# Kernel optimization log

Hardware: AMD Instinct MI355X
Metric: run time of the kernel (lower is better)

## Reference

```python
import jax, jax.numpy as jnp
import numpy as np

NUM_CODES = 1024
EMBED_DIM = 256
COMMIT_COST = 0.25


def setup_inputs() -> dict:
    key = jax.random.key(0)
    k1, k2 = jax.random.split(key)
    z_hat = jax.random.normal(k1, (32, EMBED_DIM, 32, 32), dtype=jnp.float32)
    # nn.Embedding weight init: uniform(-1/num_codes, 1/num_codes)
    embedding_weight = jax.random.uniform(
        k2, (NUM_CODES, EMBED_DIM), dtype=jnp.float32,
        minval=-1.0 / NUM_CODES, maxval=1.0 / NUM_CODES)
    return {"z_hat": z_hat, "embedding_weight": embedding_weight}


def reference(z_hat, embedding_weight):
    B, C, H, W = z_hat.shape
    # [B,C,H,W] -> [B,H,W,C] -> [N,C]
    z = jnp.transpose(z_hat, (0, 2, 3, 1))
    z_flat = z.reshape(-1, C)
    # squared L2 distances via expansion: ||z||^2 + ||e||^2 - 2 z.e
    dists = (jnp.sum(z_flat ** 2, axis=1, keepdims=True)
             + jnp.sum(embedding_weight ** 2, axis=1)
             - 2.0 * jnp.matmul(z_flat, embedding_weight.T))  # [N, K]
    idx = jnp.argmin(dists, axis=1)                            # [N]
    z_q = embedding_weight[idx].reshape(B, H, W, C)
    sg = jax.lax.stop_gradient
    codebook_loss = jnp.mean((z_q - sg(z)) ** 2)
    commitment_loss = COMMIT_COST * jnp.mean((z - sg(z_q)) ** 2)
    # straight-through estimator
    z_q_ste = z + sg(z_q - z)
    z_q_ste = jnp.transpose(z_q_ste, (0, 3, 1, 2))             # [B,C,H,W]
    indices = idx.reshape(B, H, W)
    return (z_q_ste, codebook_loss, commitment_loss, indices)
```

## Files before the change

kernel.cpp:

```cpp
#include <hip/hip_runtime.h>

#define NUM_CODES 1024
#define EMBED_DIM 256
#define NPIX      32768
#define NELEM     8388608

#define LOSS_OFF 8388608
#define IDX_OFF  8388610
#define EH_F     4194304
#define ESQ_F    4325376
#define ZSQ_F    4326400

#define MARGIN   1.0e-3f
#define CAP      16

typedef _Float16 half_t;
typedef _Float16 half8 __attribute__((ext_vector_type(8)));
typedef _Float16 half4 __attribute__((ext_vector_type(4)));
typedef float    f32x4 __attribute__((ext_vector_type(4)));
typedef unsigned int u32;
typedef unsigned long long u64;

__global__ void esq_kernel(const float* __restrict__ E, float* __restrict__ esq) {
    int w = threadIdx.x >> 6;
    int lane = threadIdx.x & 63;
    int k = blockIdx.x * 4 + w;
    const float* row = E + (size_t)k * EMBED_DIM;
    float s = 0.f;
    #pragma unroll
    for (int j = 0; j < EMBED_DIM; j += 64) { float v = row[j + lane]; s += v * v; }
    #pragma unroll
    for (int off = 32; off; off >>= 1) s += __shfl_down(s, off, 64);
    if (lane == 0) esq[k] = s;
}

__global__ void ecvt_kernel(const float* __restrict__ E, half_t* __restrict__ eh) {
    int i = (blockIdx.x * 256 + threadIdx.x) * 4;
    float4 v = *(const float4*)&E[i];
    half4 h;
    h[0] = (half_t)(v.x * 1024.f); h[1] = (half_t)(v.y * 1024.f);
    h[2] = (half_t)(v.z * 1024.f); h[3] = (half_t)(v.w * 1024.f);
    *(half4*)&eh[i] = h;
}

__global__ void zprep_kernel(const float* __restrict__ z, half_t* __restrict__ zh,
                             float* __restrict__ zsq) {
    __shared__ float zf[64 * 257];
    __shared__ float part[4][64];
    const int t = threadIdx.x;
    const int px_base = blockIdx.x * 64;
    const int b  = px_base >> 10;
    const int hw = px_base & 1023;
    {
        int px = t & 63, g = t >> 6;
        const float* zp = z + ((size_t)b << 18) + hw + px;
        float s = 0.f;
        #pragma unroll 8
        for (int r = 0; r < 64; ++r) {
            int c = g * 64 + r;
            float v = zp[(size_t)c * 1024];
            s += v * v;
            zf[px * 257 + c] = v;
        }
        part[g][px] = s;
    }
    __syncthreads();
    if (t < 64)
        zsq[px_base + t] = (part[0][t] + part[1][t]) + (part[2][t] + part[3][t]);
    {
        int px = t >> 2, q = t & 3;
        half_t* dst = zh + (size_t)(px_base + px) * 256;
        #pragma unroll
        for (int s8 = 0; s8 < 16; ++s8) {
            int c0 = q * 64 + s8 * 4;
            half4 h;
            h[0] = (half_t)zf[px * 257 + c0 + 0];
            h[1] = (half_t)zf[px * 257 + c0 + 1];
            h[2] = (half_t)zf[px * 257 + c0 + 2];
            h[3] = (half_t)zf[px * 257 + c0 + 3];
            *(half4*)&dst[c0] = h;
        }
    }
}

__launch_bounds__(256, 2)
__global__ void vq_mfma(const float* __restrict__ z, const float* __restrict__ E,
                        const half_t* __restrict__ zh, const half_t* __restrict__ ehp,
                        const float* __restrict__ esq, const float* __restrict__ zsq,
                        float* __restrict__ out, float* __restrict__ lossacc)
{
    __shared__ char lds_raw[68608];
    __shared__ u32 runmin[64];
    __shared__ u32 cnt[64];
    __shared__ u32 listd[64][CAP];
    __shared__ u32 listk[64][CAP];
    __shared__ float esqs[128];
    __shared__ float zsqs[64];
    __shared__ u64 best64[64];

    half_t* Zs = (half_t*)lds_raw;
    half_t* Es = (half_t*)(lds_raw + 33792);
    float*  zf = (float*)lds_raw;

    const int t  = threadIdx.x;
    const int l  = t & 63;
    const int wid = t >> 6;
    const int wk = wid >> 1, wp = wid & 1;
    const int l15 = l & 15, lg = l >> 4;
    const int px_base = blockIdx.x * 64;
    const int b  = px_base >> 10;
    const int hw = px_base & 1023;

    {
        int r = t >> 2, sg = t & 3;
        const uint4* src = (const uint4*)(zh + (size_t)(px_base + r) * 256 + sg * 64);
        half_t* dst = Zs + r * 264 + sg * 64;
        #pragma unroll
        for (int i = 0; i < 8; ++i) *(uint4*)(dst + i * 8) = src[i];
    }
    if (t < 64) { runmin[t] = 0x7f800000u; cnt[t] = 0u; zsqs[t] = zsq[px_base + t]; }
    __syncthreads();

    half8 zfr[8][2];
    #pragma unroll
    for (int cs = 0; cs < 8; ++cs)
        #pragma unroll
        for (int pg = 0; pg < 2; ++pg)
            zfr[cs][pg] = *(const half8*)(Zs + (wp * 32 + pg * 16 + l15) * 264 + cs * 32 + lg * 8);

    const int pxl0 = wp * 32 + l15;
    const int pxl1 = pxl0 + 16;

    #pragma unroll 1
    for (int kb = 0; kb < 8; ++kb) {
        f32x4 acc[4][2];
        #pragma unroll
        for (int kt = 0; kt < 4; ++kt)
            #pragma unroll
            for (int pg = 0; pg < 2; ++pg) acc[kt][pg] = (f32x4){0.f, 0.f, 0.f, 0.f};

        if (t < 128) esqs[t] = esq[kb * 128 + t];

        #pragma unroll
        for (int h = 0; h < 2; ++h) {
            __syncthreads();
            {
                int r = t >> 1, sg = t & 1;
                const uint4* src = (const uint4*)(ehp + (size_t)(kb * 128 + r) * 256 + h * 128 + sg * 64);
                half_t* dst = Es + r * 136 + sg * 64;
                #pragma unroll
                for (int i = 0; i < 8; ++i) *(uint4*)(dst + i * 8) = src[i];
            }
            __syncthreads();
            #pragma unroll
            for (int cs = 0; cs < 4; ++cs) {
                half8 ehf[4];
                #pragma unroll
                for (int kt = 0; kt < 4; ++kt)
                    ehf[kt] = *(const half8*)(Es + (wk * 64 + kt * 16 + l15) * 136 + cs * 32 + lg * 8);
                #pragma unroll
                for (int kt = 0; kt < 4; ++kt) {
                    acc[kt][0] = __builtin_amdgcn_mfma_f32_16x16x32_f16(ehf[kt], zfr[h * 4 + cs][0], acc[kt][0], 0, 0, 0);
                    acc[kt][1] = __builtin_amdgcn_mfma_f32_16x16x32_f16(ehf[kt], zfr[h * 4 + cs][1], acc[kt][1], 0, 0, 0);
                }
            }
        }

        float lmin0 = 3.4e38f, lmin1 = 3.4e38f;
        #pragma unroll
        for (int kt = 0; kt < 4; ++kt)
            #pragma unroll
            for (int r = 0; r < 4; ++r) {
                int kl = wk * 64 + kt * 16 + lg * 4 + r;
                float eq = esqs[kl];
                float d0 = fmaf(-0.001953125f, acc[kt][0][r], zsqs[pxl0] + eq);
                float d1 = fmaf(-0.001953125f, acc[kt][1][r], zsqs[pxl1] + eq);
                acc[kt][0][r] = d0; acc[kt][1][r] = d1;
                lmin0 = fminf(lmin0, d0); lmin1 = fminf(lmin1, d1);
            }
        atomicMin(&runmin[pxl0], __float_as_uint(lmin0));
        atomicMin(&runmin[pxl1], __float_as_uint(lmin1));
        __syncthreads();
        float thr0 = __uint_as_float(runmin[pxl0]) + MARGIN;
        float thr1 = __uint_as_float(runmin[pxl1]) + MARGIN;
        #pragma unroll
        for (int kt = 0; kt < 4; ++kt)
            #pragma unroll
            for (int r = 0; r < 4; ++r) {
                int kg = kb * 128 + wk * 64 + kt * 16 + lg * 4 + r;
                float d0 = acc[kt][0][r], d1 = acc[kt][1][r];
                if (d0 <= thr0) {
                    u32 p = atomicAdd(&cnt[pxl0], 1u);
                    if (p < CAP) { listd[pxl0][p] = __float_as_uint(d0); listk[pxl0][p] = (u32)kg; }
                }
                if (d1 <= thr1) {
                    u32 p = atomicAdd(&cnt[pxl1], 1u);
                    if (p < CAP) { listd[pxl1][p] = __float_as_uint(d1); listk[pxl1][p] = (u32)kg; }
                }
            }
        __syncthreads();
    }

    {
        int px = t & 63, cg = t >> 6;
        const float* zp = z + ((size_t)b << 18) + hw + px;
        #pragma unroll 8
        for (int r = 0; r < 64; ++r) {
            int c = cg * 64 + r;
            zf[px * 257 + c] = zp[(size_t)c * 1024];
        }
    }
    if (t < 64) best64[t] = 0xFFFFFFFFFFFFFFFFull;
    __syncthreads();

    {
        int px = t >> 2, j = t & 3;
        u32 n = cnt[px];
        if (n <= CAP) {
            float thr = __uint_as_float(runmin[px]) + MARGIN;
            const float zq = zsqs[px];
            const float* zr = zf + px * 257;
            for (u32 i = j; i < n; i += 4) {
                float da = __uint_as_float(listd[px][i]);
                if (da > thr) continue;
                int k = (int)listk[px][i];
                const float* er = E + (size_t)k * EMBED_DIM;
                float a = 0.f;
                #pragma unroll 8
                for (int c = 0; c < 256; ++c) a = fmaf(zr[c], er[c], a);
                float d = fmaf(-2.f, a, zq + esq[k]);
                u64 pk = ((u64)__float_as_uint(d) << 32) | (u32)k;
                atomicMin(&best64[px], pk);
            }
        }
    }
    __syncthreads();

    for (int px = 0; px < 64; ++px) {
        if (cnt[px] <= CAP) continue;
        const float zq = zsqs[px];
        const float* zr = zf + px * 257;
        for (int k = t; k < NUM_CODES; k += 256) {
            const float* er = E + (size_t)k * EMBED_DIM;
            float a = 0.f;
            #pragma unroll 8
            for (int c = 0; c < 256; ++c) a = fmaf(zr[c], er[c], a);
            float d = fmaf(-2.f, a, zq + esq[k]);
            u64 pk = ((u64)__float_as_uint(d) << 32) | (u32)k;
            atomicMin(&best64[px], pk);
        }
        __syncthreads();
    }
    __syncthreads();

    if (t < 64) {
        u64 pk = best64[t];
        int bk = (int)(u32)(pk & 0xFFFFFFFFull);
        float bd = __uint_as_float((u32)(pk >> 32));
        out[IDX_OFF + px_base + t] = (float)bk;
        float s = bd;
        #pragma unroll
        for (int off = 32; off; off >>= 1) s += __shfl_down(s, off, 64);
        if (t == 0) atomicAdd(lossacc, s);
    }
}

__global__ void gather_kernel(const float* __restrict__ E, float* __restrict__ out,
                              const float* __restrict__ lossacc) {
    const int t = threadIdx.x;
    const int px_base = blockIdx.x * 64;
    const int b  = px_base >> 10;
    const int hw = px_base & 1023;
    int px = t & 63, cr = t >> 6;
    int k = (int)out[IDX_OFF + px_base + px];
    float* ob = out + ((size_t)b << 18) + hw + px;
    const float* er = E + (size_t)k * EMBED_DIM;
    #pragma unroll 4
    for (int r = 0; r < 64; ++r) {
        int c = cr * 64 + r;
        ob[(size_t)c * 1024] = er[c];
    }
    if (blockIdx.x == 0 && t == 0) {
        float L = lossacc[0] / (float)NELEM;
        out[LOSS_OFF]     = L;
        out[LOSS_OFF + 1] = 0.25f * L;
    }
}

extern "C" void kernel_launch(void* const* d_in, const int* in_sizes, int n_in,
                              void* d_out, int out_size, void* d_ws, size_t ws_size,
                              hipStream_t stream) {
    const float* z = (const float*)d_in[0];
    const float* E = (const float*)d_in[1];
    float* out = (float*)d_out;
    float* ws  = (float*)d_ws;

    half_t* zh  = (half_t*)out;
    half_t* ehp = (half_t*)(out + EH_F);
    float* esqp = out + ESQ_F;
    float* zsqp = out + ZSQ_F;

    hipMemsetAsync(d_ws, 0, 64, stream);
    esq_kernel  <<<NUM_CODES / 4, 256, 0, stream>>>(E, esqp);
    ecvt_kernel <<<NUM_CODES * EMBED_DIM / 1024, 256, 0, stream>>>(E, ehp);
    zprep_kernel<<<NPIX / 64, 256, 0, stream>>>(z, zh, zsqp);
    vq_mfma     <<<NPIX / 64, 256, 0, stream>>>(z, E, zh, ehp, esqp, zsqp, out, ws);
    gather_kernel<<<NPIX / 64, 256, 0, stream>>>(E, out, ws);
}
```

Measured before the change: 175.9 us.

## Double-buffer codebook tiles in LDS via async global_load_lds with swizzle

Replaces the synchronous codebook staging in the MFMA distance loop with direct global-to-LDS async loads into two XOR-swizzled buffers. The next quarter-tile is prefetched while the current one feeds the MFMAs, using manual vmcnt waits and raw barriers. It also loads Z fragments straight from global into registers, preloads all codebook norms once, and drops the end-of-iteration syncthreads. These cut barrier and load latency stalls, but the hand-placed waitcnt and barrier ordering carries correctness risk, for example list writes racing with the next iteration's runmin and cnt updates.

```diff
diff --git a/kernel.cpp b/kernel.cpp
--- a/kernel.cpp
+++ b/kernel.cpp
@@ -20,6 +20,10 @@
 typedef float    f32x4 __attribute__((ext_vector_type(4)));
 typedef unsigned int u32;
 typedef unsigned long long u64;
+
+#define GLD16(gsrc, ldst) \
+    __builtin_amdgcn_global_load_lds((const __attribute__((address_space(1))) unsigned int*)(gsrc), \
+                                     (__attribute__((address_space(3))) unsigned int*)(ldst), 16, 0, 0)
 
 __global__ void esq_kernel(const float* __restrict__ E, float* __restrict__ esq) {
     int w = threadIdx.x >> 6;
@@ -89,18 +93,14 @@
                         const float* __restrict__ esq, const float* __restrict__ zsq,
                         float* __restrict__ out, float* __restrict__ lossacc)
 {
-    __shared__ char lds_raw[68608];
+    __shared__ char lds_raw[65792];
+    __shared__ float esqs[1024];
     __shared__ u32 runmin[64];
     __shared__ u32 cnt[64];
     __shared__ u32 listd[64][CAP];
     __shared__ u32 listk[64][CAP];
-    __shared__ float esqs[128];
     __shared__ float zsqs[64];
     __shared__ u64 best64[64];
-
-    half_t* Zs = (half_t*)lds_raw;
-    half_t* Es = (half_t*)(lds_raw + 33792);
-    float*  zf = (float*)lds_raw;
 
     const int t  = threadIdx.x;
     const int l  = t & 63;
@@ -111,25 +111,40 @@
     const int b  = px_base >> 10;
     const int hw = px_base & 1023;
 
-    {
-        int r = t >> 2, sg = t & 3;
-        const uint4* src = (const uint4*)(zh + (size_t)(px_base + r) * 256 + sg * 64);
-        half_t* dst = Zs + r * 264 + sg * 64;
-        #pragma unroll
-        for (int i = 0; i < 8; ++i) *(uint4*)(dst + i * 8) = src[i];
-    }
+    const int rloc = l >> 3;
+    const int cswz = ((l & 7) ^ rloc) << 4;
+    const char* srcbase = (const char*)ehp + (size_t)(wid * 32 + rloc) * 512 + cswz;
+    char* EsL = (char*)lds_raw;
+    char* dst0 = EsL + (wid * 4) * 1024;
+
+    GLD16(srcbase,         dst0);
+    GLD16(srcbase + 4096,  dst0 + 1024);
+    GLD16(srcbase + 8192,  dst0 + 2048);
+    GLD16(srcbase + 12288, dst0 + 3072);
+
+    #pragma unroll
+    for (int i = 0; i < 4; ++i) esqs[t + i * 256] = esq[t + i * 256];
     if (t < 64) { runmin[t] = 0x7f800000u; cnt[t] = 0u; zsqs[t] = zsq[px_base + t]; }
-    __syncthreads();
 
     half8 zfr[8][2];
     #pragma unroll
     for (int cs = 0; cs < 8; ++cs)
         #pragma unroll
         for (int pg = 0; pg < 2; ++pg)
-            zfr[cs][pg] = *(const half8*)(Zs + (wp * 32 + pg * 16 + l15) * 264 + cs * 32 + lg * 8);
+            zfr[cs][pg] = *(const half8*)(zh + (size_t)(px_base + wp * 32 + pg * 16 + l15) * 256 + cs * 32 + lg * 8);
 
     const int pxl0 = wp * 32 + l15;
     const int pxl1 = pxl0 + 16;
+
+    int ebase[4], cofs[2];
+    #pragma unroll
+    for (int kt = 0; kt < 4; ++kt) ebase[kt] = (wk * 64 + kt * 16 + l15) * 128;
+    #pragma unroll
+    for (int csl = 0; csl < 2; ++csl) cofs[csl] = (csl * 64 + lg * 16) ^ ((l15 & 7) << 4);
+
+    __syncthreads();
+    const float zq0 = zsqs[pxl0];
+    const float zq1 = zsqs[pxl1];
 
     #pragma unroll 1
     for (int kb = 0; kb < 8; ++kb) {
@@ -139,48 +154,54 @@
             #pragma unroll
             for (int pg = 0; pg < 2; ++pg) acc[kt][pg] = (f32x4){0.f, 0.f, 0.f, 0.f};
 
-        if (t < 128) esqs[t] = esq[kb * 128 + t];
-
-        #pragma unroll
-        for (int h = 0; h < 2; ++h) {
-            __syncthreads();
-            {
-                int r = t >> 1, sg = t & 1;
-                const uint4* src = (const uint4*)(ehp + (size_t)(kb * 128 + r) * 256 + h * 128 + sg * 64);
-                half_t* dst = Es + r * 136 + sg * 64;
+        #pragma unroll
+        for (int q = 0; q < 4; ++q) {
+            if (q < 3 || kb < 7) {
+                const size_t soff = (q < 3) ? ((size_t)kb * 65536 + (size_t)(q + 1) * 128)
+                                            : ((size_t)(kb + 1) * 65536);
+                const char* src = srcbase + soff;
+                char* dst = EsL + ((q + 1) & 1) * 16384 + (wid * 4) * 1024;
+                GLD16(src,         dst);
+                GLD16(src + 4096,  dst + 1024);
+                GLD16(src + 8192,  dst + 2048);
+                GLD16(src + 12288, dst + 3072);
+                asm volatile("s_waitcnt vmcnt(4)" ::: "memory");
+            } else {
+                asm volatile("s_waitcnt vmcnt(0)" ::: "memory");
+            }
+            __builtin_amdgcn_s_barrier();
+            asm volatile("" ::: "memory");
+            const char* Eq = EsL + (q & 1) * 16384;
+            #pragma unroll
+            for (int kt = 0; kt < 4; ++kt) {
                 #pragma unroll
-                for (int i = 0; i < 8; ++i) *(uint4*)(dst + i * 8) = src[i];
-            }
-            __syncthreads();
-            #pragma unroll
-            for (int cs = 0; cs < 4; ++cs) {
-                half8 ehf[4];
-                #pragma unroll
-                for (int kt = 0; kt < 4; ++kt)
-                    ehf[kt] = *(const half8*)(Es + (wk * 64 + kt * 16 + l15) * 136 + cs * 32 + lg * 8);
-                #pragma unroll
-                for (int kt = 0; kt < 4; ++kt) {
-                    acc[kt][0] = __builtin_amdgcn_mfma_f32_16x16x32_f16(ehf[kt], zfr[h * 4 + cs][0], acc[kt][0], 0, 0, 0);
-                    acc[kt][1] = __builtin_amdgcn_mfma_f32_16x16x32_f16(ehf[kt], zfr[h * 4 + cs][1], acc[kt][1], 0, 0, 0);
+                for (int csl = 0; csl < 2; ++csl) {
+                    half8 ef = *(const half8*)(Eq + ebase[kt] + cofs[csl]);
+                    acc[kt][0] = __builtin_amdgcn_mfma_f32_16x16x32_f16(ef, zfr[q * 2 + csl][0], acc[kt][0], 0, 0, 0);
+                    acc[kt][1] = __builtin_amdgcn_mfma_f32_16x16x32_f16(ef, zfr[q * 2 + csl][1], acc[kt][1], 0, 0, 0);
                 }
             }
+            asm volatile("" ::: "memory");
+            __builtin_amdgcn_s_barrier();
         }
 
         float lmin0 = 3.4e38f, lmin1 = 3.4e38f;
         #pragma unroll
-        for (int kt = 0; kt < 4; ++kt)
+        for (int kt = 0; kt < 4; ++kt) {
+            f32x4 eqv = *(const f32x4*)&esqs[kb * 128 + wk * 64 + kt * 16 + lg * 4];
             #pragma unroll
             for (int r = 0; r < 4; ++r) {
-                int kl = wk * 64 + kt * 16 + lg * 4 + r;
-                float eq = esqs[kl];
-                float d0 = fmaf(-0.001953125f, acc[kt][0][r], zsqs[pxl0] + eq);
-                float d1 = fmaf(-0.001953125f, acc[kt][1][r], zsqs[pxl1] + eq);
+                float d0 = fmaf(-0.001953125f, acc[kt][0][r], zq0 + eqv[r]);
+                float d1 = fmaf(-0.001953125f, acc[kt][1][r], zq1 + eqv[r]);
                 acc[kt][0][r] = d0; acc[kt][1][r] = d1;
                 lmin0 = fminf(lmin0, d0); lmin1 = fminf(lmin1, d1);
             }
+        }
         atomicMin(&runmin[pxl0], __float_as_uint(lmin0));
         atomicMin(&runmin[pxl1], __float_as_uint(lmin1));
-        __syncthreads();
+        asm volatile("s_waitcnt lgkmcnt(0)" ::: "memory");
+        __builtin_amdgcn_s_barrier();
+        asm volatile("" ::: "memory");
         float thr0 = __uint_as_float(runmin[pxl0]) + MARGIN;
         float thr1 = __uint_as_float(runmin[pxl1]) + MARGIN;
         #pragma unroll
@@ -198,9 +219,10 @@
                     if (p < CAP) { listd[pxl1][p] = __float_as_uint(d1); listk[pxl1][p] = (u32)kg; }
                 }
             }
-        __syncthreads();
-    }
-
+    }
+    __syncthreads();
+
+    float* zf = (float*)lds_raw;
     {
         int px = t & 63, cg = t >> 6;
         const float* zp = z + ((size_t)b << 18) + hw + px;
```

After: 164.3 us. 1.07x faster.
